# Performance work log

Measured on AMD Instinct MI355X. Metric: run time of the kernel, lower is better.

Reference implementation:

```python
import jax, jax.numpy as jnp
import numpy as np

N_EDGES = 1_250_000
N_NODES = 100_000
EDGE_DIM = 64
N_RADIAL = 16
OUT_DIM = 1


def setup_inputs() -> dict:
    key = jax.random.key(0)
    ks = jax.random.split(key, 12)
    s_e = 1.0 / np.sqrt(EDGE_DIM)
    s_r = 1.0 / np.sqrt(N_RADIAL)
    return {
        "x": jax.random.normal(ks[0], (N_EDGES, EDGE_DIM), jnp.float32),
        "rbf": jax.random.uniform(ks[1], (N_EDGES, N_RADIAL), jnp.float32),
        "idx_i": jax.random.randint(ks[2], (N_EDGES,), 0, N_NODES, jnp.int64),
        "num_nodes": N_NODES,
        # rbf_dense: Dense(n_radial, edge_dim, bias=False) -> weight (edge_dim, n_radial)
        "W_rbf": jax.random.normal(ks[3], (EDGE_DIM, N_RADIAL), jnp.float32) * s_r,
        # three hidden Dense(edge_dim, edge_dim) with bias
        "W1": jax.random.normal(ks[4], (EDGE_DIM, EDGE_DIM), jnp.float32) * s_e,
        "b1": jnp.zeros((EDGE_DIM,), jnp.float32),
        "W2": jax.random.normal(ks[5], (EDGE_DIM, EDGE_DIM), jnp.float32) * s_e,
        "b2": jnp.zeros((EDGE_DIM,), jnp.float32),
        "W3": jax.random.normal(ks[6], (EDGE_DIM, EDGE_DIM), jnp.float32) * s_e,
        "b3": jnp.zeros((EDGE_DIM,), jnp.float32),
        # final Dense(edge_dim, out_dim, bias=False) -> weight (out_dim, edge_dim)
        "W_out": jax.random.normal(ks[7], (OUT_DIM, EDGE_DIM), jnp.float32) * s_e,
    }


def swish(h):
    # Swish(beta=1.0): h * sigmoid(h)
    return h * jax.nn.sigmoid(h)


def reference(x, rbf, idx_i, num_nodes, W_rbf, W1, b1, W2, b2, W3, b3, W_out):
    # edge gating: Dense(rbf) * x  -> (n_edge, edge_dim)
    e = (rbf @ W_rbf.T) * x
    # scatter-add edges to center nodes -> (n_node, edge_dim)
    h = jax.ops.segment_sum(e, idx_i, num_segments=num_nodes)
    h = swish(h @ W1.T + b1)
    h = swish(h @ W2.T + b2)
    h = swish(h @ W3.T + b3)
    return h @ W_out.T
```

## Files before the change

kernel.cpp:

```cpp
#include <hip/hip_runtime.h>
#include <hip/hip_bf16.h>
#include <cstdint>


__global__ __launch_bounds__(256) void edge_kernel(
    const float* __restrict__ x,
    const float* __restrict__ rbf,
    const int*   __restrict__ idx,
    const float* __restrict__ Wrbf,
    float* __restrict__ hacc,
    int n_edges, int n_nodes)
{
    const int lane   = threadIdx.x & 63;
    const int wave   = blockIdx.x * (blockDim.x >> 6) + (threadIdx.x >> 6);
    const int nwaves = gridDim.x * (blockDim.x >> 6);

    float w[16];
    {
        const float4* wp = (const float4*)(Wrbf + (size_t)lane * 16);
        float4 a = wp[0], b = wp[1], c = wp[2], d = wp[3];
        w[0]=a.x; w[1]=a.y; w[2]=a.z; w[3]=a.w;
        w[4]=b.x; w[5]=b.y; w[6]=b.z; w[7]=b.w;
        w[8]=c.x; w[9]=c.y; w[10]=c.z; w[11]=c.w;
        w[12]=d.x; w[13]=d.y; w[14]=d.z; w[15]=d.w;
    }

    for (int e = wave; e < n_edges; e += nwaves) {
        const int node = idx[e];
        const float4* rp = (const float4*)(rbf + (size_t)e * 16);
        float4 r0 = rp[0], r1 = rp[1], r2 = rp[2], r3 = rp[3];
        float rv[16] = { r0.x, r0.y, r0.z, r0.w,
                         r1.x, r1.y, r1.z, r1.w,
                         r2.x, r2.y, r2.z, r2.w,
                         r3.x, r3.y, r3.z, r3.w };

        float g = 0.0f;
#pragma unroll
        for (int r = 0; r < 16; ++r) g = fmaf(rv[r], w[r], g);

        const float xv = x[(size_t)e * 64 + lane];
        if ((unsigned)node < (unsigned)n_nodes) {
            atomicAdd(&hacc[(size_t)node * 64 + lane], g * xv);
        }
    }
}

__device__ __forceinline__ float mlp_layer(const float* __restrict__ WT,
                                           const float* __restrict__ bias,
                                           float h, int lane)
{
    float acc = bias[lane];
#pragma unroll
    for (int k = 0; k < 64; ++k) {
        const float wk = WT[k * 64 + lane];
        const float hk = __int_as_float(
            __builtin_amdgcn_readlane(__float_as_int(h), k));
        acc = fmaf(wk, hk, acc);
    }
    return acc / (1.0f + __expf(-acc));
}

__global__ __launch_bounds__(256) void node_kernel(
    const float* __restrict__ hacc,
    const float* __restrict__ W1, const float* __restrict__ b1,
    const float* __restrict__ W2, const float* __restrict__ b2,
    const float* __restrict__ W3, const float* __restrict__ b3,
    const float* __restrict__ Wout,
    float* __restrict__ out,
    int n_nodes)
{
    __shared__ float WT[3][64 * 64];
    __shared__ float bs[3][64];
    __shared__ float wo[64];

    const int t = threadIdx.x;
    for (int i = t; i < 64 * 64; i += 256) {
        const int d = i & 63;
        const int k = i >> 6;
        WT[0][k * 64 + d] = W1[d * 64 + k];
        WT[1][k * 64 + d] = W2[d * 64 + k];
        WT[2][k * 64 + d] = W3[d * 64 + k];
    }
    if (t < 64) {
        bs[0][t] = b1[t];
        bs[1][t] = b2[t];
        bs[2][t] = b3[t];
        wo[t]    = Wout[t];
    }
    __syncthreads();

    const int lane   = t & 63;
    const int wave   = blockIdx.x * (blockDim.x >> 6) + (t >> 6);
    const int nwaves = gridDim.x * (blockDim.x >> 6);

    for (int node = wave; node < n_nodes; node += nwaves) {
        float h = hacc[(size_t)node * 64 + lane];
        h = mlp_layer(WT[0], bs[0], h, lane);
        h = mlp_layer(WT[1], bs[1], h, lane);
        h = mlp_layer(WT[2], bs[2], h, lane);

        float v = wo[lane] * h;
#pragma unroll
        for (int off = 32; off >= 1; off >>= 1) v += __shfl_xor(v, off, 64);

        if (lane == 0) out[node] = v;
    }
}

extern "C" void kernel_launch(void* const* d_in, const int* in_sizes, int n_in,
                              void* d_out, int out_size, void* d_ws, size_t ws_size,
                              hipStream_t stream)
{
    const float* x    = (const float*)d_in[0];
    const float* rbf  = (const float*)d_in[1];
    const int*   idx  = (const int*)d_in[2];
    const float* Wrbf = (const float*)d_in[4];
    const float* W1   = (const float*)d_in[5];
    const float* b1   = (const float*)d_in[6];
    const float* W2   = (const float*)d_in[7];
    const float* b2   = (const float*)d_in[8];
    const float* W3   = (const float*)d_in[9];
    const float* b3   = (const float*)d_in[10];
    const float* Wout = (const float*)d_in[11];

    const int n_edges = in_sizes[0] / 64;
    const int n_nodes = out_size;

    float* hacc = (float*)d_ws;

    hipMemsetAsync(hacc, 0, (size_t)n_nodes * 64 * sizeof(float), stream);

    edge_kernel<<<8192, 256, 0, stream>>>(x, rbf, idx, Wrbf, hacc,
                                          n_edges, n_nodes);

    node_kernel<<<2048, 256, 0, stream>>>(hacc, W1, b1, W2, b2, W3, b3, Wout,
                                          (float*)d_out, n_nodes);
}
```

Measured before the change: 855.6 us.

## Replace float atomics with CSR sort-by-node and fused gather-MLP kernel

Per-edge float atomic scatter-add is replaced by a counting sort of edges by destination node: histogram, single-block prefix scan, and an atomic scatter that builds an edge order. A fused node kernel then gathers each node's edges, computes the rbf gating and accumulates in registers before running the MLP, removing the 25.6 MB accumulator buffer and its memset. The cost is random gathers of x and rbf rows in the node kernel, a serial single-block scan, and extra int atomics. The removed bounds check on idx and the now non-deterministic edge order within a segment are further risks.

Result: slower. 1.614 ms (+88.7%).

```diff
diff --git a/kernel.cpp b/kernel.cpp
--- a/kernel.cpp
+++ b/kernel.cpp
@@ -3,45 +3,58 @@
 #include <cstdint>
 
 
-__global__ __launch_bounds__(256) void edge_kernel(
-    const float* __restrict__ x,
-    const float* __restrict__ rbf,
-    const int*   __restrict__ idx,
-    const float* __restrict__ Wrbf,
-    float* __restrict__ hacc,
-    int n_edges, int n_nodes)
+__global__ __launch_bounds__(256) void hist_kernel(
+    const int* __restrict__ idx, int* __restrict__ counts, int n_edges)
 {
-    const int lane   = threadIdx.x & 63;
-    const int wave   = blockIdx.x * (blockDim.x >> 6) + (threadIdx.x >> 6);
-    const int nwaves = gridDim.x * (blockDim.x >> 6);
+    int e = blockIdx.x * 256 + threadIdx.x;
+    const int stride = gridDim.x * 256;
+    for (; e < n_edges; e += stride) {
+        atomicAdd(&counts[idx[e]], 1);
+    }
+}
 
-    float w[16];
-    {
-        const float4* wp = (const float4*)(Wrbf + (size_t)lane * 16);
-        float4 a = wp[0], b = wp[1], c = wp[2], d = wp[3];
-        w[0]=a.x; w[1]=a.y; w[2]=a.z; w[3]=a.w;
-        w[4]=b.x; w[5]=b.y; w[6]=b.z; w[7]=b.w;
-        w[8]=c.x; w[9]=c.y; w[10]=c.z; w[11]=c.w;
-        w[12]=d.x; w[13]=d.y; w[14]=d.z; w[15]=d.w;
+__global__ __launch_bounds__(1024) void scan_kernel(
+    const int* __restrict__ counts,
+    int* __restrict__ offsets,
+    int* __restrict__ cursor,
+    int n)
+{
+    __shared__ int sdata[1024];
+    const int t = threadIdx.x;
+    const int chunk = (n + 1023) >> 10;
+    const int lo = t * chunk;
+    const int hi = min(lo + chunk, n);
+
+    int s = 0;
+    for (int i = lo; i < hi; ++i) s += counts[i];
+
+    sdata[t] = s;
+    __syncthreads();
+    for (int off = 1; off < 1024; off <<= 1) {
+        int v = (t >= off) ? sdata[t - off] : 0;
+        __syncthreads();
+        sdata[t] += v;
+        __syncthreads();
     }
+    int running = sdata[t] - s;
+    for (int i = lo; i < hi; ++i) {
+        const int c = counts[i];
+        offsets[i] = running;
+        cursor[i]  = running;
+        running += c;
+    }
+    if (t == 1023) offsets[n] = sdata[1023];
+}
 
-    for (int e = wave; e < n_edges; e += nwaves) {
-        const int node = idx[e];
-        const float4* rp = (const float4*)(rbf + (size_t)e * 16);
-        float4 r0 = rp[0], r1 = rp[1], r2 = rp[2], r3 = rp[3];
-        float rv[16] = { r0.x, r0.y, r0.z, r0.w,
-                         r1.x, r1.y, r1.z, r1.w,
-                         r2.x, r2.y, r2.z, r2.w,
-                         r3.x, r3.y, r3.z, r3.w };
-
-        float g = 0.0f;
-#pragma unroll
-        for (int r = 0; r < 16; ++r) g = fmaf(rv[r], w[r], g);
-
-        const float xv = x[(size_t)e * 64 + lane];
-        if ((unsigned)node < (unsigned)n_nodes) {
-            atomicAdd(&hacc[(size_t)node * 64 + lane], g * xv);
-        }
+__global__ __launch_bounds__(256) void scatter_kernel(
+    const int* __restrict__ idx, int* __restrict__ cursor,
+    int* __restrict__ edge_order, int n_edges)
+{
+    int e = blockIdx.x * 256 + threadIdx.x;
+    const int stride = gridDim.x * 256;
+    for (; e < n_edges; e += stride) {
+        const int pos = atomicAdd(&cursor[idx[e]], 1);
+        edge_order[pos] = e;
     }
 }
 
@@ -60,8 +73,12 @@
     return acc / (1.0f + __expf(-acc));
 }
 
-__global__ __launch_bounds__(256) void node_kernel(
-    const float* __restrict__ hacc,
+__global__ __launch_bounds__(256) void node_fused_kernel(
+    const float* __restrict__ x,
+    const float* __restrict__ rbf,
+    const int*   __restrict__ offsets,
+    const int*   __restrict__ edge_order,
+    const float* __restrict__ Wrbf,
     const float* __restrict__ W1, const float* __restrict__ b1,
     const float* __restrict__ W2, const float* __restrict__ b2,
     const float* __restrict__ W3, const float* __restrict__ b3,
@@ -87,14 +104,47 @@
         bs[2][t] = b3[t];
         wo[t]    = Wout[t];
     }
+
+    const int lane = t & 63;
+    float w[16];
+    {
+        const float4* wp = (const float4*)(Wrbf + (size_t)lane * 16);
+        float4 a = wp[0], b = wp[1], c = wp[2], d = wp[3];
+        w[0]=a.x; w[1]=a.y; w[2]=a.z; w[3]=a.w;
+        w[4]=b.x; w[5]=b.y; w[6]=b.z; w[7]=b.w;
+        w[8]=c.x; w[9]=c.y; w[10]=c.z; w[11]=c.w;
+        w[12]=d.x; w[13]=d.y; w[14]=d.z; w[15]=d.w;
+    }
     __syncthreads();
 
-    const int lane   = t & 63;
     const int wave   = blockIdx.x * (blockDim.x >> 6) + (t >> 6);
     const int nwaves = gridDim.x * (blockDim.x >> 6);
 
     for (int node = wave; node < n_nodes; node += nwaves) {
-        float h = hacc[(size_t)node * 64 + lane];
+        const int start = offsets[node];
+        const int end   = offsets[node + 1];
+
+        float acc = 0.0f;
+        for (int i = start; i < end; ++i) {
+            const int e = edge_order[i];
+            const float4* rp = (const float4*)(rbf + (size_t)e * 16);
+            float4 r0 = rp[0], r1 = rp[1], r2 = rp[2], r3 = rp[3];
+            const float xv = x[(size_t)e * 64 + lane];
+
+            float g = 0.0f;
+            g = fmaf(r0.x, w[0], g);  g = fmaf(r0.y, w[1], g);
+            g = fmaf(r0.z, w[2], g);  g = fmaf(r0.w, w[3], g);
+            g = fmaf(r1.x, w[4], g);  g = fmaf(r1.y, w[5], g);
+            g = fmaf(r1.z, w[6], g);  g = fmaf(r1.w, w[7], g);
+            g = fmaf(r2.x, w[8], g);  g = fmaf(r2.y, w[9], g);
+            g = fmaf(r2.z, w[10], g); g = fmaf(r2.w, w[11], g);
+            g = fmaf(r3.x, w[12], g); g = fmaf(r3.y, w[13], g);
+            g = fmaf(r3.z, w[14], g); g = fmaf(r3.w, w[15], g);
+
+            acc = fmaf(g, xv, acc);
+        }
+
+        float h = acc;
         h = mlp_layer(WT[0], bs[0], h, lane);
         h = mlp_layer(WT[1], bs[1], h, lane);
         h = mlp_layer(WT[2], bs[2], h, lane);
@@ -126,13 +176,18 @@
     const int n_edges = in_sizes[0] / 64;
     const int n_nodes = out_size;
 
-    float* hacc = (float*)d_ws;
+    int* cursor     = (int*)d_ws;
+    int* offsets    = cursor + n_nodes;
+    int* edge_order = offsets + n_nodes + 1;
 
-    hipMemsetAsync(hacc, 0, (size_t)n_nodes * 64 * sizeof(float), stream);
+    hipMemsetAsync(cursor, 0, (size_t)n_nodes * sizeof(int), stream);
 
-    edge_kernel<<<8192, 256, 0, stream>>>(x, rbf, idx, Wrbf, hacc,
-                                          n_edges, n_nodes);
+    const int eblocks = (n_edges + 255) / 256;
+    hist_kernel<<<eblocks, 256, 0, stream>>>(idx, cursor, n_edges);
+    scan_kernel<<<1, 1024, 0, stream>>>(cursor, offsets, cursor, n_nodes);
+    scatter_kernel<<<eblocks, 256, 0, stream>>>(idx, cursor, edge_order, n_edges);
 
-    node_kernel<<<2048, 256, 0, stream>>>(hacc, W1, b1, W2, b2, W3, b3, Wout,
-                                          (float*)d_out, n_nodes);
+    node_fused_kernel<<<768, 256, 0, stream>>>(
+        x, rbf, offsets, edge_order, Wrbf,
+        W1, b1, W2, b2, W3, b3, Wout, (float*)d_out, n_nodes);
 }
```
